# Performance work log

Measured on AMD Instinct MI355X. Metric: run time of the kernel, lower is better.

## Reference

```python
import jax, jax.numpy as jnp
import numpy as np

N_NODES = 50000
N_EDGES = 800000


def _gcn_norm(edge_index, n_nodes):
    # add self loops, compute symmetric normalization coefficients (PyG GCNConv)
    loop = jnp.arange(n_nodes, dtype=edge_index.dtype)
    src = jnp.concatenate([edge_index[0], loop])
    dst = jnp.concatenate([edge_index[1], loop])
    deg = jax.ops.segment_sum(jnp.ones_like(dst, dtype=jnp.float32), dst, num_segments=n_nodes)
    dinv = jnp.where(deg > 0, jax.lax.rsqrt(deg), 0.0)
    coef = dinv[src] * dinv[dst]  # [E + N]
    return src, dst, coef


def _gcn_conv(x, src, dst, coef, W, b, n_nodes):
    h = x @ W                                   # [N, out]
    msg = h[src] * coef[:, None]                # gather + scale
    agg = jax.ops.segment_sum(msg, dst, num_segments=n_nodes)
    return agg + b


def setup_inputs() -> dict:
    key = jax.random.key(0)
    ks = jax.random.split(key, 10)
    d_in, d_hid, d_out = 128, 512, 256
    num_class = [30, 25, 20, 3000]
    inp = {
        "x": jax.random.normal(ks[0], (N_NODES, d_in), dtype=jnp.float32),
        "edge_index": jax.random.randint(ks[1], (2, N_EDGES), 0, N_NODES, dtype=jnp.int64),
        "W1": jax.random.normal(ks[2], (d_in, d_hid), dtype=jnp.float32) / np.sqrt(d_in),
        "b1": jnp.zeros((d_hid,), dtype=jnp.float32),
        "W2": jax.random.normal(ks[3], (d_hid, d_out), dtype=jnp.float32) / np.sqrt(d_hid),
        "b2": jnp.zeros((d_out,), dtype=jnp.float32),
        "Wt": jax.random.normal(ks[4], (d_out, num_class[0]), dtype=jnp.float32) / np.sqrt(d_out),
        "bt": jnp.zeros((num_class[0],), dtype=jnp.float32),
        "Ws": jax.random.normal(ks[5], (d_out, num_class[1]), dtype=jnp.float32) / np.sqrt(d_out),
        "bs": jnp.zeros((num_class[1],), dtype=jnp.float32),
        "Wf": jax.random.normal(ks[6], (d_out, num_class[2]), dtype=jnp.float32) / np.sqrt(d_out),
        "bf": jnp.zeros((num_class[2],), dtype=jnp.float32),
        "Wa": jax.random.normal(ks[7], (d_out, num_class[3]), dtype=jnp.float32) / np.sqrt(d_out),
        "ba": jnp.zeros((num_class[3],), dtype=jnp.float32),
    }
    return inp


def reference(x, edge_index, W1, b1, W2, b2, Wt, bt, Ws, bs, Wf, bf, Wa, ba):
    n = x.shape[0]
    src, dst, coef = _gcn_norm(edge_index, n)
    h = jax.nn.relu(_gcn_conv(x, src, dst, coef, W1, b1, n))
    # dropout is identity at eval time
    g = _gcn_conv(h, src, dst, coef, W2, b2, n)  # graph embedding [N, 256]
    out_type = g @ Wt + bt
    out_school = g @ Ws + bs
    out_time = g @ Wf + bf
    out_author = g @ Wa + ba
    return (out_type, out_school, out_time, out_author)
```

## Files before the change

kernel.cpp:

```cpp
#include <hip/hip_runtime.h>

#define N_NODES 50000
#define N_EDGES 800000

typedef __attribute__((ext_vector_type(8))) short short8;
typedef __attribute__((ext_vector_type(4))) float f32x4;
typedef __attribute__((ext_vector_type(4))) unsigned short u16x4;

__device__ inline unsigned short f2b(float f) {
  union { float f; unsigned int u; } c; c.f = f;
  unsigned int u = c.u;
  u += 0x7FFF + ((u >> 16) & 1);
  return (unsigned short)(u >> 16);
}
__device__ inline float b2f_lo(unsigned int u) {
  union { unsigned int u; float f; } c; c.u = u << 16; return c.f;
}
__device__ inline float b2f_hi(unsigned int u) {
  union { unsigned int u; float f; } c; c.u = u & 0xFFFF0000u; return c.f;
}


__global__ void k_deg(const int* __restrict__ ei, int* __restrict__ deg) {
  int e = blockIdx.x * 256 + threadIdx.x;
  if (e < N_EDGES) atomicAdd(&deg[ei[N_EDGES + e]], 1);
}

__global__ void k_dinv(const int* __restrict__ deg, float* __restrict__ dinv) {
  int n = blockIdx.x * 256 + threadIdx.x;
  if (n < N_NODES) dinv[n] = rsqrtf((float)(deg[n] + 1));
}

__global__ void k_scan(const int* __restrict__ cnt, int* __restrict__ rowptr) {
  __shared__ int wsum[16];
  int tid = threadIdx.x, lane = tid & 63, wv = tid >> 6;
  int carry = 0;
  for (int base = 0; base < N_NODES; base += 1024) {
    int i = base + tid;
    int v = (i < N_NODES) ? cnt[i] : 0;
    int s = v;
#pragma unroll
    for (int off = 1; off < 64; off <<= 1) {
      int u = __shfl_up(s, off, 64);
      if (lane >= off) s += u;
    }
    if (lane == 63) wsum[wv] = s;
    __syncthreads();
    int ws = (lane < 16) ? wsum[lane] : 0;
#pragma unroll
    for (int off = 1; off < 16; off <<= 1) {
      int u = __shfl_up(ws, off, 64);
      if (lane >= off && lane < 16) ws += u;
    }
    int wOff = (wv == 0) ? 0 : __shfl(ws, wv - 1, 64);
    int total = __shfl(ws, 15, 64);
    if (i < N_NODES) rowptr[i] = carry + wOff + (s - v);
    carry += total;
    __syncthreads();
  }
  if (tid == 0) rowptr[N_NODES] = carry;
}

__global__ void k_fill(const int* __restrict__ ei, const int* __restrict__ rowptr,
                       int* __restrict__ cur, int* __restrict__ csr) {
  int e = blockIdx.x * 256 + threadIdx.x;
  if (e < N_EDGES) {
    int d = ei[N_EDGES + e];
    int p = atomicAdd(&cur[d], 1);
    csr[rowptr[d] + p] = ei[e];
  }
}

__global__ void k_cvt(const float* __restrict__ x, unsigned short* __restrict__ xb) {
  int i = blockIdx.x * 256 + threadIdx.x;
  const float4* x4 = (const float4*)x;
  if (i < N_NODES * 128 / 4) {
    float4 v = x4[i];
    ushort4 o; o.x = f2b(v.x); o.y = f2b(v.y); o.z = f2b(v.z); o.w = f2b(v.w);
    ((ushort4*)xb)[i] = o;
  }
}


__global__ void k_packW(const float* __restrict__ W, unsigned short* __restrict__ Bp,
                        int KS, int N) {
  int idx = blockIdx.x * 256 + threadIdx.x;
  int units = ((N + 127) / 128) * KS * 512;
  if (idx >= units) return;
  int grp = idx & 3, col = (idx >> 2) & 127;
  int rest = idx >> 9;
  int s = rest % KS, chunk = rest / KS;
  int gcol = chunk * 128 + col, k0 = s * 32 + grp * 8;
  unsigned short o[8];
#pragma unroll
  for (int j = 0; j < 8; ++j)
    o[j] = (gcol < N) ? f2b(W[(size_t)(k0 + j) * N + gcol]) : 0;
  *(short8*)(Bp + (size_t)idx * 8) = *(short8*)o;
}

__global__ void k_packH(const float* __restrict__ Wt, const float* __restrict__ Ws,
                        const float* __restrict__ Wf, const float* __restrict__ Wa,
                        const float* __restrict__ bt, const float* __restrict__ bs,
                        const float* __restrict__ bfv, const float* __restrict__ ba,
                        unsigned short* __restrict__ Bp, float* __restrict__ bcat) {
  int idx = blockIdx.x * 256 + threadIdx.x;
  const int KS = 8;
  if (idx < 102400) {
    int grp = idx & 3, col = (idx >> 2) & 127;
    int rest = idx >> 9;
    int s = rest % KS, chunk = rest / KS;
    int gcol = chunk * 128 + col, k0 = s * 32 + grp * 8;
    const float* W = Wt; int ld = 30, c = 0;
    bool ok = true;
    if (gcol < 30)                        { W = Wt; ld = 30;   c = gcol; }
    else if (gcol < 55)                   { W = Ws; ld = 25;   c = gcol - 30; }
    else if (gcol < 75)                   { W = Wf; ld = 20;   c = gcol - 55; }
    else if (gcol >= 76 && gcol < 3076)   { W = Wa; ld = 3000; c = gcol - 76; }
    else                                  { ok = false; }
    unsigned short o[8];
#pragma unroll
    for (int j = 0; j < 8; ++j)
      o[j] = ok ? f2b(W[(size_t)(k0 + j) * ld + c]) : 0;
    *(short8*)(Bp + (size_t)idx * 8) = *(short8*)o;
  }
  if (idx < 3200) {
    float v = 0.f;
    if (idx < 30)                      v = bt[idx];
    else if (idx < 55)                 v = bs[idx - 30];
    else if (idx < 75)                 v = bfv[idx - 55];
    else if (idx >= 76 && idx < 3076)  v = ba[idx - 76];
    bcat[idx] = v;
  }
}


__global__ void k_agg1(const unsigned short* __restrict__ xb, const float* __restrict__ dinv,
                       const int* __restrict__ rowptr, const int* __restrict__ csr,
                       unsigned short* __restrict__ A1) {
  int n = blockIdx.x * 4 + (threadIdx.x >> 6);
  if (n >= N_NODES) return;
  int l = threadIdx.x & 63;
  float dn = dinv[n];
  const unsigned int* x2 = (const unsigned int*)xb;
  unsigned int sv = x2[(size_t)n * 64 + l];
  float a0 = b2f_lo(sv) * dn * dn, a1 = b2f_hi(sv) * dn * dn;
  int e = rowptr[n], e1 = rowptr[n + 1];
  for (; e + 4 <= e1; e += 4) {
    int s0 = csr[e], s1 = csr[e + 1], s2 = csr[e + 2], s3 = csr[e + 3];
    float c0 = dinv[s0] * dn, c1 = dinv[s1] * dn, c2 = dinv[s2] * dn, c3 = dinv[s3] * dn;
    unsigned int v0 = x2[(size_t)s0 * 64 + l];
    unsigned int v1 = x2[(size_t)s1 * 64 + l];
    unsigned int v2 = x2[(size_t)s2 * 64 + l];
    unsigned int v3 = x2[(size_t)s3 * 64 + l];
    a0 += b2f_lo(v0) * c0 + b2f_lo(v1) * c1 + b2f_lo(v2) * c2 + b2f_lo(v3) * c3;
    a1 += b2f_hi(v0) * c0 + b2f_hi(v1) * c1 + b2f_hi(v2) * c2 + b2f_hi(v3) * c3;
  }
  for (; e < e1; ++e) {
    int s = csr[e];
    float c = dinv[s] * dn;
    unsigned int v = x2[(size_t)s * 64 + l];
    a0 += b2f_lo(v) * c; a1 += b2f_hi(v) * c;
  }
  unsigned int pk = (unsigned int)f2b(a0) | ((unsigned int)f2b(a1) << 16);
  ((unsigned int*)A1)[(size_t)n * 64 + l] = pk;
}

__global__ void k_agg2(const unsigned short* __restrict__ t, const float* __restrict__ dinv,
                       const int* __restrict__ rowptr, const int* __restrict__ csr,
                       const float* __restrict__ b2, unsigned short* __restrict__ g) {
  int n = blockIdx.x * 4 + (threadIdx.x >> 6);
  if (n >= N_NODES) return;
  int l = threadIdx.x & 63;
  float dn = dinv[n];
  const uint2* t4 = (const uint2*)t;
  uint2 sv = t4[(size_t)n * 64 + l];
  float a0 = b2f_lo(sv.x) * dn * dn, a1 = b2f_hi(sv.x) * dn * dn;
  float a2 = b2f_lo(sv.y) * dn * dn, a3 = b2f_hi(sv.y) * dn * dn;
  int e = rowptr[n], e1 = rowptr[n + 1];
  for (; e + 4 <= e1; e += 4) {
    int s0 = csr[e], s1 = csr[e + 1], s2 = csr[e + 2], s3 = csr[e + 3];
    float c0 = dinv[s0] * dn, c1 = dinv[s1] * dn, c2 = dinv[s2] * dn, c3 = dinv[s3] * dn;
    uint2 v0 = t4[(size_t)s0 * 64 + l];
    uint2 v1 = t4[(size_t)s1 * 64 + l];
    uint2 v2 = t4[(size_t)s2 * 64 + l];
    uint2 v3 = t4[(size_t)s3 * 64 + l];
    a0 += b2f_lo(v0.x) * c0 + b2f_lo(v1.x) * c1 + b2f_lo(v2.x) * c2 + b2f_lo(v3.x) * c3;
    a1 += b2f_hi(v0.x) * c0 + b2f_hi(v1.x) * c1 + b2f_hi(v2.x) * c2 + b2f_hi(v3.x) * c3;
    a2 += b2f_lo(v0.y) * c0 + b2f_lo(v1.y) * c1 + b2f_lo(v2.y) * c2 + b2f_lo(v3.y) * c3;
    a3 += b2f_hi(v0.y) * c0 + b2f_hi(v1.y) * c1 + b2f_hi(v2.y) * c2 + b2f_hi(v3.y) * c3;
  }
  for (; e < e1; ++e) {
    int s = csr[e];
    float c = dinv[s] * dn;
    uint2 v = t4[(size_t)s * 64 + l];
    a0 += b2f_lo(v.x) * c; a1 += b2f_hi(v.x) * c;
    a2 += b2f_lo(v.y) * c; a3 += b2f_hi(v.y) * c;
  }
  int d0 = l * 4;
  a0 += b2[d0]; a1 += b2[d0 + 1]; a2 += b2[d0 + 2]; a3 += b2[d0 + 3];
  ushort4 o; o.x = f2b(a0); o.y = f2b(a1); o.z = f2b(a2); o.w = f2b(a3);
  ((ushort4*)g)[(size_t)n * 64 + l] = o;
}


template <int KSTEPS, int NCHUNKS, int EPI>
__global__ __launch_bounds__(256)
void gemm_c(const unsigned short* __restrict__ A, const unsigned short* __restrict__ Bp,
            const float* __restrict__ bias, void* __restrict__ out, int M, int npanels) {
  __shared__ float lt[32][132];
  const int K = KSTEPS * 32;
  int nwg = npanels * NCHUNKS;
  int orig = blockIdx.x;
  int q = nwg >> 3, r = nwg & 7, xcd = orig & 7;
  int l = (xcd < r ? xcd * (q + 1) : r * (q + 1) + (xcd - r) * q) + (orig >> 3);
  int panel = l / NCHUNKS, chunk = l - panel * NCHUNKS;
  int tid = threadIdx.x, lane = tid & 63, w = tid >> 6;
  int ln = lane & 15, grp = lane >> 4;
  int row0 = panel * 64;

  int arow[4];
#pragma unroll
  for (int m = 0; m < 4; ++m) {
    int gr = row0 + m * 16 + ln;
    arow[m] = gr < M ? gr : M - 1;
  }

  f32x4 acc[4][2];
  f32x4 z = {0.f, 0.f, 0.f, 0.f};
#pragma unroll
  for (int m = 0; m < 4; ++m) { acc[m][0] = z; acc[m][1] = z; }

#pragma unroll 4
  for (int s = 0; s < KSTEPS; ++s) {
    short8 bfr[2];
#pragma unroll
    for (int n = 0; n < 2; ++n) {
      size_t unit = ((size_t)(chunk * KSTEPS + s) * 128 + (w * 32 + n * 16 + ln)) * 4 + grp;
      bfr[n] = *(const short8*)(Bp + unit * 8);
    }
    short8 am[4];
#pragma unroll
    for (int m = 0; m < 4; ++m)
      am[m] = *(const short8*)(A + (size_t)arow[m] * K + s * 32 + grp * 8);
#pragma unroll
    for (int m = 0; m < 4; ++m)
#pragma unroll
      for (int n = 0; n < 2; ++n)
        acc[m][n] = __builtin_amdgcn_mfma_f32_16x16x32_bf16(am[m], bfr[n], acc[m][n], 0, 0, 0);
  }

  int c0 = chunk * 128;
  float bv[2];
#pragma unroll
  for (int n = 0; n < 2; ++n)
    bv[n] = (EPI == 1) ? 0.f : bias[c0 + w * 32 + n * 16 + ln];

#pragma unroll
  for (int half = 0; half < 2; ++half) {
    if (half) __syncthreads();
#pragma unroll
    for (int n = 0; n < 2; ++n) {
#pragma unroll
      for (int mm = 0; mm < 2; ++mm) {
        int m = half * 2 + mm;
#pragma unroll
        for (int rr = 0; rr < 4; ++rr) {
          float v = acc[m][n][rr] + bv[n];
          if (EPI == 0) v = v > 0.f ? v : 0.f;
          lt[mm * 16 + grp * 4 + rr][w * 32 + n * 16 + ln] = v;
        }
      }
    }
    __syncthreads();

    int col4 = tid & 31, rowi = tid >> 5;
#pragma unroll
    for (int rr = 0; rr < 4; ++rr) {
      int rw = rr * 8 + rowi;
      int grow = row0 + half * 32 + rw;
      if (grow >= M) continue;
      f32x4 v = *(const f32x4*)&lt[rw][col4 * 4];
      if (EPI == 2) {
        int gcn0 = c0 + col4 * 4;
        float* o = (float*)out;
        if (gcn0 >= 76 && gcn0 + 4 <= 3076) {
          __builtin_nontemporal_store(v, (f32x4*)(o + 3750000ull + (size_t)grow * 3000 + (gcn0 - 76)));
        } else {
#pragma unroll
          for (int j = 0; j < 4; ++j) {
            int gcn = gcn0 + j;
            if (gcn >= 3076) continue;
            size_t offo;
            if (gcn < 30)      offo = (size_t)grow * 30 + gcn;
            else if (gcn < 55) offo = 1500000ull + (size_t)grow * 25 + (gcn - 30);
            else if (gcn < 75) offo = 2750000ull + (size_t)grow * 20 + (gcn - 55);
            else if (gcn == 75) continue;
            else               offo = 3750000ull + (size_t)grow * 3000 + (gcn - 76);
            o[offo] = v[j];
          }
        }
      } else {
        const int NOUT = NCHUNKS * 128;
        u16x4 b;
        b[0] = f2b(v[0]); b[1] = f2b(v[1]); b[2] = f2b(v[2]); b[3] = f2b(v[3]);
        *(u16x4*)((unsigned short*)out + (size_t)grow * NOUT + c0 + col4 * 4) = b;
      }
    }
  }
}


extern "C" void kernel_launch(void* const* d_in, const int* in_sizes, int n_in,
                              void* d_out, int out_size, void* d_ws, size_t ws_size,
                              hipStream_t stream) {
  const float* x  = (const float*)d_in[0];
  const int* ei   = (const int*)d_in[1];
  const float* W1 = (const float*)d_in[2];
  const float* b1 = (const float*)d_in[3];
  const float* W2 = (const float*)d_in[4];
  const float* b2 = (const float*)d_in[5];
  const float* Wt = (const float*)d_in[6];
  const float* bt = (const float*)d_in[7];
  const float* Ws = (const float*)d_in[8];
  const float* bs = (const float*)d_in[9];
  const float* Wf = (const float*)d_in[10];
  const float* bf_ = (const float*)d_in[11];
  const float* Wa = (const float*)d_in[12];
  const float* ba = (const float*)d_in[13];

  char* ws = (char*)d_ws;
  size_t off = 0;
  auto alloc = [&](size_t bytes) {
    void* p = ws + off;
    off = (off + bytes + 255) & ~(size_t)255;
    return p;
  };
  int* deg    = (int*)alloc(N_NODES * 4);
  int* cur    = (int*)alloc(N_NODES * 4);
  float* dinv = (float*)alloc(N_NODES * 4);
  int* rowptr = (int*)alloc((N_NODES + 1) * 4);
  int* csr    = (int*)alloc((size_t)N_EDGES * 4);
  unsigned short* xb = (unsigned short*)alloc((size_t)N_NODES * 128 * 2);
  unsigned short* A1 = (unsigned short*)alloc((size_t)N_NODES * 128 * 2);
  unsigned short* h  = (unsigned short*)alloc((size_t)N_NODES * 512 * 2);
  unsigned short* t  = (unsigned short*)alloc((size_t)N_NODES * 256 * 2);
  unsigned short* g  = h;
  unsigned short* Bp0 = (unsigned short*)alloc((size_t)512 * 128 * 2);
  unsigned short* Bp1 = (unsigned short*)alloc((size_t)256 * 512 * 2);
  unsigned short* BpH = (unsigned short*)alloc((size_t)3200 * 256 * 2);
  float* bcat = (float*)alloc(3200 * 4);

  const int NP = (N_NODES + 63) / 64;

  hipMemsetAsync(deg, 0, N_NODES * 4, stream);
  hipMemsetAsync(cur, 0, N_NODES * 4, stream);
  k_deg<<<(N_EDGES + 255) / 256, 256, 0, stream>>>(ei, deg);
  k_dinv<<<(N_NODES + 255) / 256, 256, 0, stream>>>(deg, dinv);
  k_scan<<<1, 1024, 0, stream>>>(deg, rowptr);
  k_fill<<<(N_EDGES + 255) / 256, 256, 0, stream>>>(ei, rowptr, cur, csr);
  k_cvt<<<(N_NODES * 128 / 4 + 255) / 256, 256, 0, stream>>>(x, xb);
  k_packW<<<(512 * 128 / 8 + 255) / 256, 256, 0, stream>>>(W1, Bp0, 4, 512);
  k_packW<<<(256 * 512 / 8 + 255) / 256, 256, 0, stream>>>(W2, Bp1, 16, 256);
  k_packH<<<(102400 + 255) / 256, 256, 0, stream>>>(Wt, Ws, Wf, Wa, bt, bs, bf_, ba, BpH, bcat);
  k_agg1<<<(N_NODES + 3) / 4, 256, 0, stream>>>(xb, dinv, rowptr, csr, A1);
  gemm_c<4, 4, 0><<<NP * 4, 256, 0, stream>>>(A1, Bp0, b1, h, N_NODES, NP);
  gemm_c<16, 2, 1><<<NP * 2, 256, 0, stream>>>(h, Bp1, nullptr, t, N_NODES, NP);
  k_agg2<<<(N_NODES + 3) / 4, 256, 0, stream>>>(t, dinv, rowptr, csr, b2, g);
  gemm_c<8, 25, 2><<<NP * 25, 256, 0, stream>>>(g, BpH, bcat, d_out, N_NODES, NP);
}
```

Measured before the change: 737.3 us.

## Replace head GEMM with row-panel kernel holding A fragments in registers

The four-head output GEMM (256 -> 3076 columns) moves from the generic tiled gemm_c to a dedicated gemm_h kernel. In gemm_h each 512-thread block takes a 16-row panel, keeps the whole K=256 A fragment in registers, and sweeps all 25 column chunks, reading B directly from global memory in a repacked column-major layout. Blocks are remapped so that each XCD handles a contiguous range of panels. The aim is to read each A row once instead of once per column tile and to stream the large fp32 output row by row. The cost is 100 accumulator registers per thread, B being re-read from L2 by every block, and a __syncthreads per chunk in the epilogue.

```diff
diff --git a/kernel.cpp b/kernel.cpp
--- a/kernel.cpp
+++ b/kernel.cpp
@@ -104,12 +104,12 @@
                         const float* __restrict__ bfv, const float* __restrict__ ba,
                         unsigned short* __restrict__ Bp, float* __restrict__ bcat) {
   int idx = blockIdx.x * 256 + threadIdx.x;
-  const int KS = 8;
   if (idx < 102400) {
-    int grp = idx & 3, col = (idx >> 2) & 127;
-    int rest = idx >> 9;
-    int s = rest % KS, chunk = rest / KS;
-    int gcol = chunk * 128 + col, k0 = s * 32 + grp * 8;
+    int grp = idx & 3;
+    int rest = idx >> 2;
+    int gcol = rest % 3200;
+    int s = rest / 3200;
+    int k0 = s * 32 + grp * 8;
     const float* W = Wt; int ld = 30, c = 0;
     bool ok = true;
     if (gcol < 30)                        { W = Wt; ld = 30;   c = gcol; }
@@ -280,30 +280,72 @@
       int grow = row0 + half * 32 + rw;
       if (grow >= M) continue;
       f32x4 v = *(const f32x4*)&lt[rw][col4 * 4];
-      if (EPI == 2) {
-        int gcn0 = c0 + col4 * 4;
-        float* o = (float*)out;
-        if (gcn0 >= 76 && gcn0 + 4 <= 3076) {
-          __builtin_nontemporal_store(v, (f32x4*)(o + 3750000ull + (size_t)grow * 3000 + (gcn0 - 76)));
-        } else {
-#pragma unroll
-          for (int j = 0; j < 4; ++j) {
-            int gcn = gcn0 + j;
-            if (gcn >= 3076) continue;
-            size_t offo;
-            if (gcn < 30)      offo = (size_t)grow * 30 + gcn;
-            else if (gcn < 55) offo = 1500000ull + (size_t)grow * 25 + (gcn - 30);
-            else if (gcn < 75) offo = 2750000ull + (size_t)grow * 20 + (gcn - 55);
-            else if (gcn == 75) continue;
-            else               offo = 3750000ull + (size_t)grow * 3000 + (gcn - 76);
-            o[offo] = v[j];
-          }
-        }
-      } else {
-        const int NOUT = NCHUNKS * 128;
-        u16x4 b;
-        b[0] = f2b(v[0]); b[1] = f2b(v[1]); b[2] = f2b(v[2]); b[3] = f2b(v[3]);
-        *(u16x4*)((unsigned short*)out + (size_t)grow * NOUT + c0 + col4 * 4) = b;
+      const int NOUT = NCHUNKS * 128;
+      u16x4 b;
+      b[0] = f2b(v[0]); b[1] = f2b(v[1]); b[2] = f2b(v[2]); b[3] = f2b(v[3]);
+      *(u16x4*)((unsigned short*)out + (size_t)grow * NOUT + c0 + col4 * 4) = b;
+    }
+  }
+}
+
+
+__global__ __launch_bounds__(512)
+void gemm_h(const unsigned short* __restrict__ A, const unsigned short* __restrict__ Bp,
+            const float* __restrict__ bias, float* __restrict__ out) {
+  __shared__ float lt[2][16][132];
+  const int nwg = N_NODES / 16;
+  int orig = blockIdx.x;
+  int q = nwg >> 3, r = nwg & 7, xcd = orig & 7;
+  int pan = (xcd < r ? xcd * (q + 1) : r * (q + 1) + (xcd - r) * q) + (orig >> 3);
+  int tid = threadIdx.x, lane = tid & 63, w = tid >> 6;
+  int ln = lane & 15, grp = lane >> 4;
+  int row0 = pan * 16;
+
+  short8 af[8];
+#pragma unroll
+  for (int s = 0; s < 8; ++s)
+    af[s] = *(const short8*)(A + (size_t)(row0 + ln) * 256 + s * 32 + grp * 8);
+
+  f32x4 acc[25];
+  f32x4 z = {0.f, 0.f, 0.f, 0.f};
+#pragma unroll
+  for (int t = 0; t < 25; ++t) acc[t] = z;
+
+#pragma unroll
+  for (int s = 0; s < 8; ++s) {
+#pragma unroll
+    for (int t = 0; t < 25; ++t) {
+      int col = t * 128 + w * 16 + ln;
+      short8 bf = *(const short8*)(Bp + ((size_t)(s * 3200 + col) * 4 + grp) * 8);
+      acc[t] = __builtin_amdgcn_mfma_f32_16x16x32_bf16(af[s], bf, acc[t], 0, 0, 0);
+    }
+  }
+
+  int col4 = tid & 31, rw = tid >> 5;
+  int grow = row0 + rw;
+#pragma unroll
+  for (int t = 0; t < 25; ++t) {
+    float bv = bias[t * 128 + w * 16 + ln];
+#pragma unroll
+    for (int rr = 0; rr < 4; ++rr)
+      lt[t & 1][grp * 4 + rr][w * 16 + ln] = acc[t][rr] + bv;
+    __syncthreads();
+    f32x4 v = *(const f32x4*)&lt[t & 1][rw][col4 * 4];
+    int gcn0 = t * 128 + col4 * 4;
+    if (gcn0 >= 76 && gcn0 + 4 <= 3076) {
+      __builtin_nontemporal_store(v, (f32x4*)(out + 3750000ull + (size_t)grow * 3000 + (gcn0 - 76)));
+    } else {
+#pragma unroll
+      for (int j = 0; j < 4; ++j) {
+        int gcn = gcn0 + j;
+        if (gcn >= 3076) continue;
+        size_t offo;
+        if (gcn < 30)      offo = (size_t)grow * 30 + gcn;
+        else if (gcn < 55) offo = 1500000ull + (size_t)grow * 25 + (gcn - 30);
+        else if (gcn < 75) offo = 2750000ull + (size_t)grow * 20 + (gcn - 55);
+        else if (gcn == 75) continue;
+        else               offo = 3750000ull + (size_t)grow * 3000 + (gcn - 76);
+        out[offo] = v[j];
       }
     }
   }
@@ -366,5 +408,5 @@
   gemm_c<4, 4, 0><<<NP * 4, 256, 0, stream>>>(A1, Bp0, b1, h, N_NODES, NP);
   gemm_c<16, 2, 1><<<NP * 2, 256, 0, stream>>>(h, Bp1, nullptr, t, N_NODES, NP);
   k_agg2<<<(N_NODES + 3) / 4, 256, 0, stream>>>(t, dinv, rowptr, csr, b2, g);
-  gemm_c<8, 25, 2><<<NP * 25, 256, 0, stream>>>(g, BpH, bcat, d_out, N_NODES, NP);
-}
+  gemm_h<<<N_NODES / 16, 512, 0, stream>>>(g, BpH, bcat, (float*)d_out);
+}
```

New measurement: 803.7 us. +9.0%, slower.
